# Kernel optimization log

Measured on AMD Instinct MI355X. Metric: run time of the kernel, lower is better.

The kernel has to match this reference:

```python
import jax, jax.numpy as jnp
import numpy as np

B, L, PATCH_IN, D, NPOS = 64, 1024, 768, 1152, 256


def setup_inputs() -> dict:
    key = jax.random.key(0)
    k1, k2, k3, k4 = jax.random.split(key, 4)
    pixel_values = jax.random.normal(k1, (B, L, PATCH_IN), dtype=jnp.float32)
    # per-sample (h, w) with h*w <= L and h, w >= 16 (pure upsampling of 16x16 grid)
    hs = np.array([16 + (i % 17) for i in range(B)], dtype=np.int64)
    ws = (L // hs).astype(np.int64)
    spatial_shapes = jnp.asarray(np.stack([hs, ws], axis=1))
    W = jax.random.normal(k2, (D, PATCH_IN), dtype=jnp.float32) * 0.02
    b = jax.random.normal(k3, (D,), dtype=jnp.float32) * 0.02
    pos_emb = jax.random.normal(k4, (NPOS, D), dtype=jnp.float32) * 0.02
    return {"pixel_values": pixel_values, "spatial_shapes": spatial_shapes,
            "W": W, "b": b, "pos_emb": pos_emb}


def _resized_pos_embeddings(pos_emb, spatial_shapes_np, max_length):
    # pos_emb: [num_patches, D] -> [G, G, D] grid
    g = int(np.sqrt(pos_emb.shape[0]))
    d = pos_emb.shape[1]
    grid = pos_emb.reshape(g, g, d)
    rows = []
    for i in range(spatial_shapes_np.shape[0]):
        h, w = int(spatial_shapes_np[i, 0]), int(spatial_shapes_np[i, 1])
        # half-pixel bilinear == torch F.interpolate(align_corners=False); antialias
        # is a no-op for upsampling (h, w >= g)
        r = jax.image.resize(grid, (h, w, d), method="bilinear").reshape(h * w, d)
        pad = jnp.broadcast_to(r[0], (max_length - h * w, d))  # replicate first patch
        rows.append(jnp.concatenate([r, pad], axis=0))
    return jnp.stack(rows)  # [B, max_length, D]


def reference(pixel_values, spatial_shapes, W, b, pos_emb):
    # patch linear embedding: [B, L, Cpp] x [D, Cpp] -> [B, L, D]
    patch_embeds = jnp.einsum("blk,dk->bld", pixel_values, W) + b
    ss = np.asarray(spatial_shapes)  # static per-sample shapes
    pos = _resized_pos_embeddings(pos_emb, ss, pixel_values.shape[1])
    return patch_embeds + pos
```

## Files before the change

kernel.cpp:

```cpp
#include <hip/hip_runtime.h>

typedef __bf16 bf16x8 __attribute__((ext_vector_type(8)));
typedef float  f32x4  __attribute__((ext_vector_type(4)));

constexpr int BM = 128, BN = 128, BK = 32;
constexpr int MDIM = 65536, NDIM = 1152, KDIM = 768;
constexpr int NBN = NDIM / BN;
constexpr int NKT = KDIM / BK;
constexpr int GRID = (MDIM / BM) * NBN;
constexpr int LDSROWB = BK * 2;


__device__ __forceinline__ void gload16(const void* g, void* l) {
  __builtin_amdgcn_global_load_lds(
      (const __attribute__((address_space(1))) void*)g,
      (__attribute__((address_space(3))) void*)l, 16, 0, 0);
}

__device__ __forceinline__ unsigned pk2(float x, float y) {
  __bf16 a = (__bf16)x, b = (__bf16)y;
  return (unsigned)__builtin_bit_cast(unsigned short, a) |
         ((unsigned)__builtin_bit_cast(unsigned short, b) << 16);
}

__global__ __launch_bounds__(256)
void repack_kernel(const float* __restrict__ in, __bf16* __restrict__ out) {
  const int c    = blockIdx.x * 256 + threadIdx.x;
  const int c_in = c & 511;
  const int img  = c >> 9;
  const int kt   = img % NKT;
  const int pan  = img / NKT;
  const int o = c_in * 16;
  const int u = (o >> 6) & 7;
  const int a = o ^ ((u ^ (u >> 2)) << 4);
  const int r = a >> 6;
  const int p = (a >> 4) & 3;
  const float* src = in + (size_t)(pan * 128 + r) * KDIM + kt * 32 + p * 8;
  const float4 x = *reinterpret_cast<const float4*>(src);
  const float4 y = *reinterpret_cast<const float4*>(src + 4);
  uint4 r4;
  r4.x = pk2(x.x, x.y); r4.y = pk2(x.z, x.w);
  r4.z = pk2(y.x, y.y); r4.w = pk2(y.z, y.w);
  *reinterpret_cast<uint4*>(out + (size_t)c * 8) = r4;
}

__global__ __launch_bounds__(256, 4)
void gemm_swz_kernel(const __bf16* __restrict__ Aimg,
                     const __bf16* __restrict__ Bimg,
                     const int*   __restrict__ ss,
                     const float* __restrict__ bias,
                     const float* __restrict__ pos,
                     float* __restrict__ out) {
  __shared__ __bf16 As[2][BM * BK];
  __shared__ __bf16 Bs[2][BM * BK];

  const int tid  = threadIdx.x;
  const int lane = tid & 63;
  const int wid  = tid >> 6;
  const int wr   = wid >> 1;
  const int wc   = wid & 1;

  const int bidh = blockIdx.x;
  const int bid  = (bidh & 7) * (GRID / 8) + (bidh >> 3);
  const int bm   = bid / NBN;
  const int bn   = bid % NBN;

  auto stage = [&](int kt, int buf) {
    const __bf16* wsA = Aimg + ((size_t)(bm * NKT + kt) << 12);
    const __bf16* wsB = Bimg + ((size_t)(bn * NKT + kt) << 12);
    gload16(wsA + tid * 8,         (char*)(&As[buf][0]) + tid * 16);
    gload16(wsA + (256 + tid) * 8, (char*)(&As[buf][0]) + (256 + tid) * 16);
    gload16(wsB + tid * 8,         (char*)(&Bs[buf][0]) + tid * 16);
    gload16(wsB + (256 + tid) * 8, (char*)(&Bs[buf][0]) + (256 + tid) * 16);
  };

  f32x4 acc[4][4];
#pragma unroll
  for (int i = 0; i < 4; ++i)
#pragma unroll
    for (int j = 0; j < 4; ++j) acc[i][j] = (f32x4)0.0f;

  const int fr = lane & 15;
  const int kg = lane >> 4;
  const int abase = (((wr * 64 + fr) * LDSROWB) + kg * 16) ^ ((fr & 7) << 4);
  const int bbase = (((wc * 64 + fr) * LDSROWB) + kg * 16) ^ ((fr & 7) << 4);

  auto compute = [&](int buf) {
    const char* pa = reinterpret_cast<const char*>(&As[buf][0]);
    const char* pb = reinterpret_cast<const char*>(&Bs[buf][0]);
    bf16x8 af[4], bfv[4];
#pragma unroll
    for (int mf = 0; mf < 4; ++mf)
      af[mf] = *reinterpret_cast<const bf16x8*>(pa + abase + mf * 16 * LDSROWB);
#pragma unroll
    for (int nf = 0; nf < 4; ++nf)
      bfv[nf] = *reinterpret_cast<const bf16x8*>(pb + bbase + nf * 16 * LDSROWB);
#pragma unroll
    for (int mf = 0; mf < 4; ++mf)
#pragma unroll
      for (int nf = 0; nf < 4; ++nf)
        acc[mf][nf] = __builtin_amdgcn_mfma_f32_16x16x32_bf16(bfv[nf], af[mf], acc[mf][nf], 0, 0, 0);
  };

  stage(0, 0);
  for (int kt = 0; kt < NKT; ++kt) {
    const int cur = kt & 1;
    __syncthreads();
    if (kt + 1 < NKT) stage(kt + 1, cur ^ 1);
    compute(cur);
  }

  const int colq = bn * BN + wc * 64 + kg * 4;
  f32x4 bias4[4];
#pragma unroll
  for (int nf = 0; nf < 4; ++nf)
    bias4[nf] = *reinterpret_cast<const f32x4*>(bias + colq + nf * 16);

  const int s  = bm >> 3;
  const int h  = ss[2 * s];
  const int w  = ss[2 * s + 1];
  const int hw = h * w;
  const float rh = 16.0f / (float)h;
  const float rw = 16.0f / (float)w;

#pragma unroll
  for (int mf = 0; mf < 4; ++mf) {
    const int row = bm * BM + wr * 64 + mf * 16 + fr;
    int p = row & 1023;
    if (p >= hw) p = 0;
    const int y = p / w;
    const int x = p - y * w;
    const float fy = ((float)y + 0.5f) * rh - 0.5f;
    const float fx = ((float)x + 0.5f) * rw - 0.5f;
    const float yf = floorf(fy), xf = floorf(fx);
    const float ty = fy - yf,   tx = fx - xf;
    int iy0 = (int)yf, ix0 = (int)xf;
    int iy1 = iy0 + 1 > 15 ? 15 : iy0 + 1;
    int ix1 = ix0 + 1 > 15 ? 15 : ix0 + 1;
    iy0 = iy0 < 0 ? 0 : iy0;
    ix0 = ix0 < 0 ? 0 : ix0;
    const float* g00 = pos + (size_t)(iy0 * 16 + ix0) * NDIM;
    const float* g01 = pos + (size_t)(iy0 * 16 + ix1) * NDIM;
    const float* g10 = pos + (size_t)(iy1 * 16 + ix0) * NDIM;
    const float* g11 = pos + (size_t)(iy1 * 16 + ix1) * NDIM;
    float* orow = out + (size_t)row * NDIM;
#pragma unroll
    for (int nf = 0; nf < 4; ++nf) {
      const int col = colq + nf * 16;
      const f32x4 v00 = *reinterpret_cast<const f32x4*>(g00 + col);
      const f32x4 v01 = *reinterpret_cast<const f32x4*>(g01 + col);
      const f32x4 v10 = *reinterpret_cast<const f32x4*>(g10 + col);
      const f32x4 v11 = *reinterpret_cast<const f32x4*>(g11 + col);
      const f32x4 top = v00 + tx * (v01 - v00);
      const f32x4 bot = v10 + tx * (v11 - v10);
      const f32x4 pv  = top + ty * (bot - top);
      *reinterpret_cast<f32x4*>(orow + col) = acc[mf][nf] + bias4[nf] + pv;
    }
  }
}

__global__ __launch_bounds__(256, 2)
void gemm_fb_kernel(const float* __restrict__ A,
                    const int*   __restrict__ ss,
                    const float* __restrict__ Wm,
                    const float* __restrict__ bias,
                    const float* __restrict__ pos,
                    float* __restrict__ out) {
  __shared__ unsigned short As[2][BM * BK];
  __shared__ unsigned short Bs[2][BM * BK];

  const int tid  = threadIdx.x;
  const int lane = tid & 63;
  const int wid  = tid >> 6;
  const int wr   = wid >> 1;
  const int wc   = wid & 1;

  const int bidh = blockIdx.x;
  const int bid  = (bidh & 7) * (GRID / 8) + (bidh >> 3);
  const int bm   = bid / NBN;
  const int bn   = bid % NBN;

  const int srow0 = tid >> 3;
  const int skc   = tid & 7;
  const float* Ag = A  + (size_t)(bm * BM + srow0) * KDIM + skc * 4;
  const float* Bg = Wm + (size_t)(bn * BN + srow0) * KDIM + skc * 4;

  float4 ra[4], rb[4];

  auto stage_load = [&](int kt) {
    const int ko = kt * BK;
#pragma unroll
    for (int r = 0; r < 4; ++r) {
      ra[r] = *reinterpret_cast<const float4*>(Ag + (size_t)(r * 32) * KDIM + ko);
      rb[r] = *reinterpret_cast<const float4*>(Bg + (size_t)(r * 32) * KDIM + ko);
    }
  };

  auto stage_write = [&](int buf) {
#pragma unroll
    for (int r = 0; r < 4; ++r) {
      const int arow = r * 32 + srow0;
      int off = arow * LDSROWB + skc * 8;
      off ^= (arow & 7) << 4;
      uint2 pa, pb;
      pa.x = pk2(ra[r].x, ra[r].y); pa.y = pk2(ra[r].z, ra[r].w);
      pb.x = pk2(rb[r].x, rb[r].y); pb.y = pk2(rb[r].z, rb[r].w);
      *reinterpret_cast<uint2*>(reinterpret_cast<char*>(&As[buf][0]) + off) = pa;
      *reinterpret_cast<uint2*>(reinterpret_cast<char*>(&Bs[buf][0]) + off) = pb;
    }
  };

  f32x4 acc[4][4];
#pragma unroll
  for (int i = 0; i < 4; ++i)
#pragma unroll
    for (int j = 0; j < 4; ++j) acc[i][j] = (f32x4)0.0f;

  const int fr = lane & 15;
  const int kg = lane >> 4;
  int abase = (wr * 64 + fr) * LDSROWB + kg * 16; abase ^= (fr & 7) << 4;
  int bbase = (wc * 64 + fr) * LDSROWB + kg * 16; bbase ^= (fr & 7) << 4;

  auto compute = [&](int buf) {
    const char* pa = reinterpret_cast<const char*>(&As[buf][0]);
    const char* pb = reinterpret_cast<const char*>(&Bs[buf][0]);
    bf16x8 af[4], bfv[4];
#pragma unroll
    for (int mf = 0; mf < 4; ++mf)
      af[mf] = *reinterpret_cast<const bf16x8*>(pa + abase + mf * 16 * LDSROWB);
#pragma unroll
    for (int nf = 0; nf < 4; ++nf)
      bfv[nf] = *reinterpret_cast<const bf16x8*>(pb + bbase + nf * 16 * LDSROWB);
#pragma unroll
    for (int mf = 0; mf < 4; ++mf)
#pragma unroll
      for (int nf = 0; nf < 4; ++nf)
        acc[mf][nf] = __builtin_amdgcn_mfma_f32_16x16x32_bf16(af[mf], bfv[nf], acc[mf][nf], 0, 0, 0);
  };

  stage_load(0);
  stage_write(0);
  for (int kt = 0; kt < NKT; ++kt) {
    const int cur = kt & 1;
    if (kt + 1 < NKT) stage_load(kt + 1);
    __syncthreads();
    compute(cur);
    if (kt + 1 < NKT) stage_write(cur ^ 1);
  }

  const int colbase = bn * BN + wc * 64 + fr;
  float bvals[4];
#pragma unroll
  for (int nf = 0; nf < 4; ++nf) bvals[nf] = bias[colbase + nf * 16];

  const int s  = bm >> 3;
  const int h  = ss[2 * s];
  const int w  = ss[2 * s + 1];
  const int hw = h * w;
  const float rh = 16.0f / (float)h;
  const float rw = 16.0f / (float)w;
  const int row0 = bm * BM + wr * 64 + kg * 4;

#pragma unroll
  for (int mf = 0; mf < 4; ++mf) {
#pragma unroll
    for (int rg = 0; rg < 4; ++rg) {
      const int row = row0 + mf * 16 + rg;
      int p = row & 1023;
      if (p >= hw) p = 0;
      const int y = p / w;
      const int x = p - y * w;
      const float fy = ((float)y + 0.5f) * rh - 0.5f;
      const float fx = ((float)x + 0.5f) * rw - 0.5f;
      const float yf = floorf(fy), xf = floorf(fx);
      const float ty = fy - yf,   tx = fx - xf;
      int iy0 = (int)yf, ix0 = (int)xf;
      int iy1 = iy0 + 1 > 15 ? 15 : iy0 + 1;
      int ix1 = ix0 + 1 > 15 ? 15 : ix0 + 1;
      iy0 = iy0 < 0 ? 0 : iy0;
      ix0 = ix0 < 0 ? 0 : ix0;
      const float* g00 = pos + (size_t)(iy0 * 16 + ix0) * NDIM;
      const float* g01 = pos + (size_t)(iy0 * 16 + ix1) * NDIM;
      const float* g10 = pos + (size_t)(iy1 * 16 + ix0) * NDIM;
      const float* g11 = pos + (size_t)(iy1 * 16 + ix1) * NDIM;
      float* orow = out + (size_t)row * NDIM;
#pragma unroll
      for (int nf = 0; nf < 4; ++nf) {
        const int col = colbase + nf * 16;
        const float p00 = g00[col], p01 = g01[col];
        const float p10 = g10[col], p11 = g11[col];
        const float top = p00 + tx * (p01 - p00);
        const float bot = p10 + tx * (p11 - p10);
        const float pv  = top + ty * (bot - top);
        orow[col] = acc[mf][nf][rg] + bvals[nf] + pv;
      }
    }
  }
}

extern "C" void kernel_launch(void* const* d_in, const int* in_sizes, int n_in,
                              void* d_out, int out_size, void* d_ws, size_t ws_size,
                              hipStream_t stream) {
  const float* A    = (const float*)d_in[0];
  const int*   ss   = (const int*)d_in[1];
  const float* Wm   = (const float*)d_in[2];
  const float* bias = (const float*)d_in[3];
  const float* pos  = (const float*)d_in[4];
  float* out = (float*)d_out;

  const size_t needA = (size_t)MDIM * KDIM * 2;
  const size_t needW = (size_t)NDIM * KDIM * 2;

  if (ws_size >= needA + needW) {
    __bf16* Ab = (__bf16*)d_ws;
    __bf16* Bb = (__bf16*)((char*)d_ws + needA);
    const int chunksA = (MDIM / 16) * NKT * 64;
    const int chunksW = (NDIM / 16) * NKT * 64;
    repack_kernel<<<chunksA / 256, 256, 0, stream>>>(A, Ab);
    repack_kernel<<<chunksW / 256, 256, 0, stream>>>(Wm, Bb);
    gemm_swz_kernel<<<GRID, 256, 0, stream>>>(Ab, Bb, ss, bias, pos, out);
  } else {
    gemm_fb_kernel<<<GRID, 256, 0, stream>>>(A, ss, Wm, bias, pos, out);
  }
}
```

Measured before the change: 291.8 us.

## Triple-buffer LDS pipeline with explicit waitcnt in repacked bf16 GEMM

Replaces the double-buffered main GEMM with a three-stage LDS ring. Two tiles are prefetched ahead, and explicit s_waitcnt vmcnt(4) plus raw s_barrier calls let one tile's loads remain in flight during compute. It also swaps the MFMA operand order and switches the epilogue to the scalar per-element layout, with base pointers hoisted. Occupancy drops to three blocks per CU to make room for the extra LDS buffer.

```diff
diff --git a/kernel.cpp b/kernel.cpp
--- a/kernel.cpp
+++ b/kernel.cpp
@@ -44,15 +44,15 @@
   *reinterpret_cast<uint4*>(out + (size_t)c * 8) = r4;
 }
 
-__global__ __launch_bounds__(256, 4)
-void gemm_swz_kernel(const __bf16* __restrict__ Aimg,
-                     const __bf16* __restrict__ Bimg,
-                     const int*   __restrict__ ss,
-                     const float* __restrict__ bias,
-                     const float* __restrict__ pos,
-                     float* __restrict__ out) {
-  __shared__ __bf16 As[2][BM * BK];
-  __shared__ __bf16 Bs[2][BM * BK];
+__global__ __launch_bounds__(256, 3)
+void gemm_pipe_kernel(const __bf16* __restrict__ Aimg,
+                      const __bf16* __restrict__ Bimg,
+                      const int*   __restrict__ ss,
+                      const float* __restrict__ bias,
+                      const float* __restrict__ pos,
+                      float* __restrict__ out) {
+  __shared__ __bf16 As[3][BM * BK];
+  __shared__ __bf16 Bs[3][BM * BK];
 
   const int tid  = threadIdx.x;
   const int lane = tid & 63;
@@ -65,9 +65,12 @@
   const int bm   = bid / NBN;
   const int bn   = bid % NBN;
 
+  const __bf16* wsA0 = Aimg + ((size_t)(bm * NKT) << 12);
+  const __bf16* wsB0 = Bimg + ((size_t)(bn * NKT) << 12);
+
   auto stage = [&](int kt, int buf) {
-    const __bf16* wsA = Aimg + ((size_t)(bm * NKT + kt) << 12);
-    const __bf16* wsB = Bimg + ((size_t)(bn * NKT + kt) << 12);
+    const __bf16* wsA = wsA0 + ((size_t)kt << 12);
+    const __bf16* wsB = wsB0 + ((size_t)kt << 12);
     gload16(wsA + tid * 8,         (char*)(&As[buf][0]) + tid * 16);
     gload16(wsA + (256 + tid) * 8, (char*)(&As[buf][0]) + (256 + tid) * 16);
     gload16(wsB + tid * 8,         (char*)(&Bs[buf][0]) + tid * 16);
@@ -99,154 +102,31 @@
     for (int mf = 0; mf < 4; ++mf)
 #pragma unroll
       for (int nf = 0; nf < 4; ++nf)
-        acc[mf][nf] = __builtin_amdgcn_mfma_f32_16x16x32_bf16(bfv[nf], af[mf], acc[mf][nf], 0, 0, 0);
+        acc[mf][nf] = __builtin_amdgcn_mfma_f32_16x16x32_bf16(af[mf], bfv[nf], acc[mf][nf], 0, 0, 0);
   };
 
   stage(0, 0);
-  for (int kt = 0; kt < NKT; ++kt) {
-    const int cur = kt & 1;
-    __syncthreads();
-    if (kt + 1 < NKT) stage(kt + 1, cur ^ 1);
+  stage(1, 1);
+  int cur = 0;
+  for (int kt = 0; kt < NKT - 1; ++kt) {
+    asm volatile("s_waitcnt vmcnt(4)" ::: "memory");
+    asm volatile("s_waitcnt lgkmcnt(0)" ::: "memory");
+    __builtin_amdgcn_sched_barrier(0);
+    __builtin_amdgcn_s_barrier();
+    __builtin_amdgcn_sched_barrier(0);
+    if (kt + 2 < NKT) {
+      const int nxt = cur >= 1 ? cur - 1 : 2;
+      stage(kt + 2, nxt);
+    }
     compute(cur);
-  }
-
-  const int colq = bn * BN + wc * 64 + kg * 4;
-  f32x4 bias4[4];
-#pragma unroll
-  for (int nf = 0; nf < 4; ++nf)
-    bias4[nf] = *reinterpret_cast<const f32x4*>(bias + colq + nf * 16);
-
-  const int s  = bm >> 3;
-  const int h  = ss[2 * s];
-  const int w  = ss[2 * s + 1];
-  const int hw = h * w;
-  const float rh = 16.0f / (float)h;
-  const float rw = 16.0f / (float)w;
-
-#pragma unroll
-  for (int mf = 0; mf < 4; ++mf) {
-    const int row = bm * BM + wr * 64 + mf * 16 + fr;
-    int p = row & 1023;
-    if (p >= hw) p = 0;
-    const int y = p / w;
-    const int x = p - y * w;
-    const float fy = ((float)y + 0.5f) * rh - 0.5f;
-    const float fx = ((float)x + 0.5f) * rw - 0.5f;
-    const float yf = floorf(fy), xf = floorf(fx);
-    const float ty = fy - yf,   tx = fx - xf;
-    int iy0 = (int)yf, ix0 = (int)xf;
-    int iy1 = iy0 + 1 > 15 ? 15 : iy0 + 1;
-    int ix1 = ix0 + 1 > 15 ? 15 : ix0 + 1;
-    iy0 = iy0 < 0 ? 0 : iy0;
-    ix0 = ix0 < 0 ? 0 : ix0;
-    const float* g00 = pos + (size_t)(iy0 * 16 + ix0) * NDIM;
-    const float* g01 = pos + (size_t)(iy0 * 16 + ix1) * NDIM;
-    const float* g10 = pos + (size_t)(iy1 * 16 + ix0) * NDIM;
-    const float* g11 = pos + (size_t)(iy1 * 16 + ix1) * NDIM;
-    float* orow = out + (size_t)row * NDIM;
-#pragma unroll
-    for (int nf = 0; nf < 4; ++nf) {
-      const int col = colq + nf * 16;
-      const f32x4 v00 = *reinterpret_cast<const f32x4*>(g00 + col);
-      const f32x4 v01 = *reinterpret_cast<const f32x4*>(g01 + col);
-      const f32x4 v10 = *reinterpret_cast<const f32x4*>(g10 + col);
-      const f32x4 v11 = *reinterpret_cast<const f32x4*>(g11 + col);
-      const f32x4 top = v00 + tx * (v01 - v00);
-      const f32x4 bot = v10 + tx * (v11 - v10);
-      const f32x4 pv  = top + ty * (bot - top);
-      *reinterpret_cast<f32x4*>(orow + col) = acc[mf][nf] + bias4[nf] + pv;
-    }
-  }
-}
-
-__global__ __launch_bounds__(256, 2)
-void gemm_fb_kernel(const float* __restrict__ A,
-                    const int*   __restrict__ ss,
-                    const float* __restrict__ Wm,
-                    const float* __restrict__ bias,
-                    const float* __restrict__ pos,
-                    float* __restrict__ out) {
-  __shared__ unsigned short As[2][BM * BK];
-  __shared__ unsigned short Bs[2][BM * BK];
-
-  const int tid  = threadIdx.x;
-  const int lane = tid & 63;
-  const int wid  = tid >> 6;
-  const int wr   = wid >> 1;
-  const int wc   = wid & 1;
-
-  const int bidh = blockIdx.x;
-  const int bid  = (bidh & 7) * (GRID / 8) + (bidh >> 3);
-  const int bm   = bid / NBN;
-  const int bn   = bid % NBN;
-
-  const int srow0 = tid >> 3;
-  const int skc   = tid & 7;
-  const float* Ag = A  + (size_t)(bm * BM + srow0) * KDIM + skc * 4;
-  const float* Bg = Wm + (size_t)(bn * BN + srow0) * KDIM + skc * 4;
-
-  float4 ra[4], rb[4];
-
-  auto stage_load = [&](int kt) {
-    const int ko = kt * BK;
-#pragma unroll
-    for (int r = 0; r < 4; ++r) {
-      ra[r] = *reinterpret_cast<const float4*>(Ag + (size_t)(r * 32) * KDIM + ko);
-      rb[r] = *reinterpret_cast<const float4*>(Bg + (size_t)(r * 32) * KDIM + ko);
-    }
-  };
-
-  auto stage_write = [&](int buf) {
-#pragma unroll
-    for (int r = 0; r < 4; ++r) {
-      const int arow = r * 32 + srow0;
-      int off = arow * LDSROWB + skc * 8;
-      off ^= (arow & 7) << 4;
-      uint2 pa, pb;
-      pa.x = pk2(ra[r].x, ra[r].y); pa.y = pk2(ra[r].z, ra[r].w);
-      pb.x = pk2(rb[r].x, rb[r].y); pb.y = pk2(rb[r].z, rb[r].w);
-      *reinterpret_cast<uint2*>(reinterpret_cast<char*>(&As[buf][0]) + off) = pa;
-      *reinterpret_cast<uint2*>(reinterpret_cast<char*>(&Bs[buf][0]) + off) = pb;
-    }
-  };
-
-  f32x4 acc[4][4];
-#pragma unroll
-  for (int i = 0; i < 4; ++i)
-#pragma unroll
-    for (int j = 0; j < 4; ++j) acc[i][j] = (f32x4)0.0f;
-
-  const int fr = lane & 15;
-  const int kg = lane >> 4;
-  int abase = (wr * 64 + fr) * LDSROWB + kg * 16; abase ^= (fr & 7) << 4;
-  int bbase = (wc * 64 + fr) * LDSROWB + kg * 16; bbase ^= (fr & 7) << 4;
-
-  auto compute = [&](int buf) {
-    const char* pa = reinterpret_cast<const char*>(&As[buf][0]);
-    const char* pb = reinterpret_cast<const char*>(&Bs[buf][0]);
-    bf16x8 af[4], bfv[4];
-#pragma unroll
-    for (int mf = 0; mf < 4; ++mf)
-      af[mf] = *reinterpret_cast<const bf16x8*>(pa + abase + mf * 16 * LDSROWB);
-#pragma unroll
-    for (int nf = 0; nf < 4; ++nf)
-      bfv[nf] = *reinterpret_cast<const bf16x8*>(pb + bbase + nf * 16 * LDSROWB);
-#pragma unroll
-    for (int mf = 0; mf < 4; ++mf)
-#pragma unroll
-      for (int nf = 0; nf < 4; ++nf)
-        acc[mf][nf] = __builtin_amdgcn_mfma_f32_16x16x32_bf16(af[mf], bfv[nf], acc[mf][nf], 0, 0, 0);
-  };
-
-  stage_load(0);
-  stage_write(0);
-  for (int kt = 0; kt < NKT; ++kt) {
-    const int cur = kt & 1;
-    if (kt + 1 < NKT) stage_load(kt + 1);
-    __syncthreads();
-    compute(cur);
-    if (kt + 1 < NKT) stage_write(cur ^ 1);
-  }
+    cur = cur < 2 ? cur + 1 : 0;
+  }
+  asm volatile("s_waitcnt vmcnt(0)" ::: "memory");
+  asm volatile("s_waitcnt lgkmcnt(0)" ::: "memory");
+  __builtin_amdgcn_sched_barrier(0);
+  __builtin_amdgcn_s_barrier();
+  __builtin_amdgcn_sched_barrier(0);
+  compute(cur);
 
   const int colbase = bn * BN + wc * 64 + fr;
   float bvals[4];
@@ -298,6 +178,145 @@
   }
 }
 
+__global__ __launch_bounds__(256, 2)
+void gemm_fb_kernel(const float* __restrict__ A,
+                    const int*   __restrict__ ss,
+                    const float* __restrict__ Wm,
+                    const float* __restrict__ bias,
+                    const float* __restrict__ pos,
+                    float* __restrict__ out) {
+  __shared__ unsigned short As[2][BM * BK];
+  __shared__ unsigned short Bs[2][BM * BK];
+
+  const int tid  = threadIdx.x;
+  const int lane = tid & 63;
+  const int wid  = tid >> 6;
+  const int wr   = wid >> 1;
+  const int wc   = wid & 1;
+
+  const int bidh = blockIdx.x;
+  const int bid  = (bidh & 7) * (GRID / 8) + (bidh >> 3);
+  const int bm   = bid / NBN;
+  const int bn   = bid % NBN;
+
+  const int srow0 = tid >> 3;
+  const int skc   = tid & 7;
+  const float* Ag = A  + (size_t)(bm * BM + srow0) * KDIM + skc * 4;
+  const float* Bg = Wm + (size_t)(bn * BN + srow0) * KDIM + skc * 4;
+
+  float4 ra[4], rb[4];
+
+  auto stage_load = [&](int kt) {
+    const int ko = kt * BK;
+#pragma unroll
+    for (int r = 0; r < 4; ++r) {
+      ra[r] = *reinterpret_cast<const float4*>(Ag + (size_t)(r * 32) * KDIM + ko);
+      rb[r] = *reinterpret_cast<const float4*>(Bg + (size_t)(r * 32) * KDIM + ko);
+    }
+  };
+
+  auto stage_write = [&](int buf) {
+#pragma unroll
+    for (int r = 0; r < 4; ++r) {
+      const int arow = r * 32 + srow0;
+      int off = arow * LDSROWB + skc * 8;
+      off ^= (arow & 7) << 4;
+      uint2 pa, pb;
+      pa.x = pk2(ra[r].x, ra[r].y); pa.y = pk2(ra[r].z, ra[r].w);
+      pb.x = pk2(rb[r].x, rb[r].y); pb.y = pk2(rb[r].z, rb[r].w);
+      *reinterpret_cast<uint2*>(reinterpret_cast<char*>(&As[buf][0]) + off) = pa;
+      *reinterpret_cast<uint2*>(reinterpret_cast<char*>(&Bs[buf][0]) + off) = pb;
+    }
+  };
+
+  f32x4 acc[4][4];
+#pragma unroll
+  for (int i = 0; i < 4; ++i)
+#pragma unroll
+    for (int j = 0; j < 4; ++j) acc[i][j] = (f32x4)0.0f;
+
+  const int fr = lane & 15;
+  const int kg = lane >> 4;
+  int abase = (wr * 64 + fr) * LDSROWB + kg * 16; abase ^= (fr & 7) << 4;
+  int bbase = (wc * 64 + fr) * LDSROWB + kg * 16; bbase ^= (fr & 7) << 4;
+
+  auto compute = [&](int buf) {
+    const char* pa = reinterpret_cast<const char*>(&As[buf][0]);
+    const char* pb = reinterpret_cast<const char*>(&Bs[buf][0]);
+    bf16x8 af[4], bfv[4];
+#pragma unroll
+    for (int mf = 0; mf < 4; ++mf)
+      af[mf] = *reinterpret_cast<const bf16x8*>(pa + abase + mf * 16 * LDSROWB);
+#pragma unroll
+    for (int nf = 0; nf < 4; ++nf)
+      bfv[nf] = *reinterpret_cast<const bf16x8*>(pb + bbase + nf * 16 * LDSROWB);
+#pragma unroll
+    for (int mf = 0; mf < 4; ++mf)
+#pragma unroll
+      for (int nf = 0; nf < 4; ++nf)
+        acc[mf][nf] = __builtin_amdgcn_mfma_f32_16x16x32_bf16(af[mf], bfv[nf], acc[mf][nf], 0, 0, 0);
+  };
+
+  stage_load(0);
+  stage_write(0);
+  for (int kt = 0; kt < NKT; ++kt) {
+    const int cur = kt & 1;
+    if (kt + 1 < NKT) stage_load(kt + 1);
+    __syncthreads();
+    compute(cur);
+    if (kt + 1 < NKT) stage_write(cur ^ 1);
+  }
+
+  const int colbase = bn * BN + wc * 64 + fr;
+  float bvals[4];
+#pragma unroll
+  for (int nf = 0; nf < 4; ++nf) bvals[nf] = bias[colbase + nf * 16];
+
+  const int s  = bm >> 3;
+  const int h  = ss[2 * s];
+  const int w  = ss[2 * s + 1];
+  const int hw = h * w;
+  const float rh = 16.0f / (float)h;
+  const float rw = 16.0f / (float)w;
+  const int row0 = bm * BM + wr * 64 + kg * 4;
+
+#pragma unroll
+  for (int mf = 0; mf < 4; ++mf) {
+#pragma unroll
+    for (int rg = 0; rg < 4; ++rg) {
+      const int row = row0 + mf * 16 + rg;
+      int p = row & 1023;
+      if (p >= hw) p = 0;
+      const int y = p / w;
+      const int x = p - y * w;
+      const float fy = ((float)y + 0.5f) * rh - 0.5f;
+      const float fx = ((float)x + 0.5f) * rw - 0.5f;
+      const float yf = floorf(fy), xf = floorf(fx);
+      const float ty = fy - yf,   tx = fx - xf;
+      int iy0 = (int)yf, ix0 = (int)xf;
+      int iy1 = iy0 + 1 > 15 ? 15 : iy0 + 1;
+      int ix1 = ix0 + 1 > 15 ? 15 : ix0 + 1;
+      iy0 = iy0 < 0 ? 0 : iy0;
+      ix0 = ix0 < 0 ? 0 : ix0;
+      const float* g00 = pos + (size_t)(iy0 * 16 + ix0) * NDIM;
+      const float* g01 = pos + (size_t)(iy0 * 16 + ix1) * NDIM;
+      const float* g10 = pos + (size_t)(iy1 * 16 + ix0) * NDIM;
+      const float* g11 = pos + (size_t)(iy1 * 16 + ix1) * NDIM;
+      float* orow = out + (size_t)row * NDIM;
+#pragma unroll
+      for (int nf = 0; nf < 4; ++nf) {
+        const int col = colbase + nf * 16;
+        const float p00 = g00[col], p01 = g01[col];
+        const float p10 = g10[col], p11 = g11[col];
+        const float top = p00 + tx * (p01 - p00);
+        const float bot = p10 + tx * (p11 - p10);
+        const float pv  = top + ty * (bot - top);
+        orow[col] = acc[mf][nf][rg] + bvals[nf] + pv;
+      }
+    }
+  }
+}
+
 extern "C" void kernel_launch(void* const* d_in, const int* in_sizes, int n_in,
                               void* d_out, int out_size, void* d_ws, size_t ws_size,
                               hipStream_t stream) {
@@ -318,7 +337,7 @@
     const int chunksW = (NDIM / 16) * NKT * 64;
     repack_kernel<<<chunksA / 256, 256, 0, stream>>>(A, Ab);
     repack_kernel<<<chunksW / 256, 256, 0, stream>>>(Wm, Bb);
-    gemm_swz_kernel<<<GRID, 256, 0, stream>>>(Ab, Bb, ss, bias, pos, out);
+    gemm_pipe_kernel<<<GRID, 256, 0, stream>>>(Ab, Bb, ss, bias, pos, out);
   } else {
     gemm_fb_kernel<<<GRID, 256, 0, stream>>>(A, ss, Wm, bias, pos, out);
   }
```

Result: slower. 306.1 us (+4.9%).

## Stage GEMM epilogue through swizzled LDS for coalesced 32-byte row stores

Applied to the files above, without the earlier changes.

The epilogue now swaps the MFMA operand order and writes the accumulator tile into shared memory, reusing the A/B staging buffers with an XOR swizzle. It then reads rows back so each thread handles 8 contiguous columns of one row. This makes global stores and pos-embedding gathers row-contiguous, and the bilinear index math runs per row chunk instead of per fragment. The cost is two extra barriers per half-tile, LDS round trips, and a lower occupancy hint (3 instead of 4 blocks per CU).

```diff
diff --git a/kernel.cpp b/kernel.cpp
--- a/kernel.cpp
+++ b/kernel.cpp
@@ -9,7 +9,6 @@
 constexpr int NKT = KDIM / BK;
 constexpr int GRID = (MDIM / BM) * NBN;
 constexpr int LDSROWB = BK * 2;
-
 
 __device__ __forceinline__ void gload16(const void* g, void* l) {
   __builtin_amdgcn_global_load_lds(
@@ -44,15 +43,17 @@
   *reinterpret_cast<uint4*>(out + (size_t)c * 8) = r4;
 }
 
-__global__ __launch_bounds__(256, 4)
-void gemm_swz_kernel(const __bf16* __restrict__ Aimg,
-                     const __bf16* __restrict__ Bimg,
-                     const int*   __restrict__ ss,
-                     const float* __restrict__ bias,
-                     const float* __restrict__ pos,
-                     float* __restrict__ out) {
-  __shared__ __bf16 As[2][BM * BK];
-  __shared__ __bf16 Bs[2][BM * BK];
+__global__ __launch_bounds__(256, 3)
+void gemm_swz2_kernel(const __bf16* __restrict__ Aimg,
+                      const __bf16* __restrict__ Bimg,
+                      const int*   __restrict__ ss,
+                      const float* __restrict__ bias,
+                      const float* __restrict__ pos,
+                      float* __restrict__ out) {
+  __shared__ __align__(16) unsigned char SM[32768];
+  __bf16* As0 = reinterpret_cast<__bf16*>(SM);
+  __bf16* Bs0 = reinterpret_cast<__bf16*>(SM + 16384);
+  float*  Cs  = reinterpret_cast<float*>(SM);
 
   const int tid  = threadIdx.x;
   const int lane = tid & 63;
@@ -68,10 +69,12 @@
   auto stage = [&](int kt, int buf) {
     const __bf16* wsA = Aimg + ((size_t)(bm * NKT + kt) << 12);
     const __bf16* wsB = Bimg + ((size_t)(bn * NKT + kt) << 12);
-    gload16(wsA + tid * 8,         (char*)(&As[buf][0]) + tid * 16);
-    gload16(wsA + (256 + tid) * 8, (char*)(&As[buf][0]) + (256 + tid) * 16);
-    gload16(wsB + tid * 8,         (char*)(&Bs[buf][0]) + tid * 16);
-    gload16(wsB + (256 + tid) * 8, (char*)(&Bs[buf][0]) + (256 + tid) * 16);
+    char* la = (char*)As0 + buf * 8192;
+    char* lb = (char*)Bs0 + buf * 8192;
+    gload16(wsA + tid * 8,         la + tid * 16);
+    gload16(wsA + (256 + tid) * 8, la + (256 + tid) * 16);
+    gload16(wsB + tid * 8,         lb + tid * 16);
+    gload16(wsB + (256 + tid) * 8, lb + (256 + tid) * 16);
   };
 
   f32x4 acc[4][4];
@@ -86,8 +89,8 @@
   const int bbase = (((wc * 64 + fr) * LDSROWB) + kg * 16) ^ ((fr & 7) << 4);
 
   auto compute = [&](int buf) {
-    const char* pa = reinterpret_cast<const char*>(&As[buf][0]);
-    const char* pb = reinterpret_cast<const char*>(&Bs[buf][0]);
+    const char* pa = (const char*)As0 + buf * 8192;
+    const char* pb = (const char*)Bs0 + buf * 8192;
     bf16x8 af[4], bfv[4];
 #pragma unroll
     for (int mf = 0; mf < 4; ++mf)
@@ -99,7 +102,7 @@
     for (int mf = 0; mf < 4; ++mf)
 #pragma unroll
       for (int nf = 0; nf < 4; ++nf)
-        acc[mf][nf] = __builtin_amdgcn_mfma_f32_16x16x32_bf16(bfv[nf], af[mf], acc[mf][nf], 0, 0, 0);
+        acc[mf][nf] = __builtin_amdgcn_mfma_f32_16x16x32_bf16(af[mf], bfv[nf], acc[mf][nf], 0, 0, 0);
   };
 
   stage(0, 0);
@@ -110,11 +113,10 @@
     compute(cur);
   }
 
-  const int colq = bn * BN + wc * 64 + kg * 4;
-  f32x4 bias4[4];
-#pragma unroll
-  for (int nf = 0; nf < 4; ++nf)
-    bias4[nf] = *reinterpret_cast<const f32x4*>(bias + colq + nf * 16);
+  const int chunk = tid & 15;
+  const int gcol  = bn * BN + chunk * 8;
+  const f32x4 bias_lo = *reinterpret_cast<const f32x4*>(bias + gcol);
+  const f32x4 bias_hi = *reinterpret_cast<const f32x4*>(bias + gcol + 4);
 
   const int s  = bm >> 3;
   const int h  = ss[2 * s];
@@ -124,37 +126,68 @@
   const float rw = 16.0f / (float)w;
 
 #pragma unroll
-  for (int mf = 0; mf < 4; ++mf) {
-    const int row = bm * BM + wr * 64 + mf * 16 + fr;
-    int p = row & 1023;
-    if (p >= hw) p = 0;
-    const int y = p / w;
-    const int x = p - y * w;
-    const float fy = ((float)y + 0.5f) * rh - 0.5f;
-    const float fx = ((float)x + 0.5f) * rw - 0.5f;
-    const float yf = floorf(fy), xf = floorf(fx);
-    const float ty = fy - yf,   tx = fx - xf;
-    int iy0 = (int)yf, ix0 = (int)xf;
-    int iy1 = iy0 + 1 > 15 ? 15 : iy0 + 1;
-    int ix1 = ix0 + 1 > 15 ? 15 : ix0 + 1;
-    iy0 = iy0 < 0 ? 0 : iy0;
-    ix0 = ix0 < 0 ? 0 : ix0;
-    const float* g00 = pos + (size_t)(iy0 * 16 + ix0) * NDIM;
-    const float* g01 = pos + (size_t)(iy0 * 16 + ix1) * NDIM;
-    const float* g10 = pos + (size_t)(iy1 * 16 + ix0) * NDIM;
-    const float* g11 = pos + (size_t)(iy1 * 16 + ix1) * NDIM;
-    float* orow = out + (size_t)row * NDIM;
-#pragma unroll
-    for (int nf = 0; nf < 4; ++nf) {
-      const int col = colq + nf * 16;
-      const f32x4 v00 = *reinterpret_cast<const f32x4*>(g00 + col);
-      const f32x4 v01 = *reinterpret_cast<const f32x4*>(g01 + col);
-      const f32x4 v10 = *reinterpret_cast<const f32x4*>(g10 + col);
-      const f32x4 v11 = *reinterpret_cast<const f32x4*>(g11 + col);
-      const f32x4 top = v00 + tx * (v01 - v00);
-      const f32x4 bot = v10 + tx * (v11 - v10);
-      const f32x4 pv  = top + ty * (bot - top);
-      *reinterpret_cast<f32x4*>(orow + col) = acc[mf][nf] + bias4[nf] + pv;
+  for (int half = 0; half < 2; ++half) {
+    __syncthreads();
+#pragma unroll
+    for (int mm = 0; mm < 2; ++mm) {
+#pragma unroll
+      for (int nf = 0; nf < 4; ++nf) {
+#pragma unroll
+        for (int rg = 0; rg < 4; ++rg) {
+          const int rowL = wr * 32 + mm * 16 + kg * 4 + rg;
+          const int col  = wc * 64 + nf * 16 + fr;
+          const int key  = (rowL & 3) ^ ((rowL >> 2) & 3);
+          Cs[(rowL << 7) + (col ^ (key << 3))] = acc[half * 2 + mm][nf][rg];
+        }
+      }
+    }
+    __syncthreads();
+#pragma unroll
+    for (int pass = 0; pass < 4; ++pass) {
+      const int rowL = pass * 16 + (tid >> 4);
+      const int key  = (rowL & 3) ^ ((rowL >> 2) & 3);
+      const float* crow = Cs + (rowL << 7) + ((chunk ^ key) << 3);
+      const f32x4 c0 = *reinterpret_cast<const f32x4*>(crow);
+      const f32x4 c1 = *reinterpret_cast<const f32x4*>(crow + 4);
+
+      const int grow = bm * BM + (rowL >> 5) * 64 + half * 32 + (rowL & 31);
+      int p = grow & 1023;
+      if (p >= hw) p = 0;
+      const int y = p / w;
+      const int x = p - y * w;
+      const float fy = ((float)y + 0.5f) * rh - 0.5f;
+      const float fx = ((float)x + 0.5f) * rw - 0.5f;
+      const float yf = floorf(fy), xf = floorf(fx);
+      const float ty = fy - yf,   tx = fx - xf;
+      int iy0 = (int)yf, ix0 = (int)xf;
+      int iy1 = iy0 + 1 > 15 ? 15 : iy0 + 1;
+      int ix1 = ix0 + 1 > 15 ? 15 : ix0 + 1;
+      iy0 = iy0 < 0 ? 0 : iy0;
+      ix0 = ix0 < 0 ? 0 : ix0;
+      const float* g00 = pos + (size_t)(iy0 * 16 + ix0) * NDIM + gcol;
+      const float* g01 = pos + (size_t)(iy0 * 16 + ix1) * NDIM + gcol;
+      const float* g10 = pos + (size_t)(iy1 * 16 + ix0) * NDIM + gcol;
+      const float* g11 = pos + (size_t)(iy1 * 16 + ix1) * NDIM + gcol;
+
+      const f32x4 v00l = *reinterpret_cast<const f32x4*>(g00);
+      const f32x4 v01l = *reinterpret_cast<const f32x4*>(g01);
+      const f32x4 v10l = *reinterpret_cast<const f32x4*>(g10);
+      const f32x4 v11l = *reinterpret_cast<const f32x4*>(g11);
+      const f32x4 v00h = *reinterpret_cast<const f32x4*>(g00 + 4);
+      const f32x4 v01h = *reinterpret_cast<const f32x4*>(g01 + 4);
+      const f32x4 v10h = *reinterpret_cast<const f32x4*>(g10 + 4);
+      const f32x4 v11h = *reinterpret_cast<const f32x4*>(g11 + 4);
+
+      const f32x4 topl = v00l + tx * (v01l - v00l);
+      const f32x4 botl = v10l + tx * (v11l - v10l);
+      const f32x4 pvl  = topl + ty * (botl - topl);
+      const f32x4 toph = v00h + tx * (v01h - v00h);
+      const f32x4 both = v10h + tx * (v11h - v10h);
+      const f32x4 pvh  = toph + ty * (both - toph);
+
+      float* orow = out + (size_t)grow * NDIM + gcol;
+      *reinterpret_cast<f32x4*>(orow)     = c0 + bias_lo + pvl;
+      *reinterpret_cast<f32x4*>(orow + 4) = c1 + bias_hi + pvh;
     }
   }
 }
@@ -318,7 +351,7 @@
     const int chunksW = (NDIM / 16) * NKT * 64;
     repack_kernel<<<chunksA / 256, 256, 0, stream>>>(A, Ab);
     repack_kernel<<<chunksW / 256, 256, 0, stream>>>(Wm, Bb);
-    gemm_swz_kernel<<<GRID, 256, 0, stream>>>(Ab, Bb, ss, bias, pos, out);
+    gemm_swz2_kernel<<<GRID, 256, 0, stream>>>(Ab, Bb, ss, bias, pos, out);
   } else {
     gemm_fb_kernel<<<GRID, 256, 0, stream>>>(A, ss, Wm, bias, pos, out);
   }
```

After: 262.8 us. 9.9% less time.
